# Optimization experiments

Hardware: AMD Instinct MI355X
Metric: run time of the kernel (lower is better)

## Reference

```python
import jax, jax.numpy as jnp
import numpy as np

STRIDES = [8, 16, 32, 64, 128]
HW = [(100, 128), (50, 64), (25, 32), (13, 16), (7, 8)]
SCORE_THR = 0.05
IOU_THR = 0.6
MAX_DET = 1000
MAX_OUT = 100  # fixed pad size in _post_process


def _coords(h, w, stride):
    # FCOS coords_fmap2orig: center of each cell in original image coords
    sx = jnp.arange(w, dtype=jnp.float32) * stride + stride // 2
    sy = jnp.arange(h, dtype=jnp.float32) * stride + stride // 2
    yy, xx = jnp.meshgrid(sy, sx, indexing='ij')
    return jnp.stack([xx.reshape(-1), yy.reshape(-1)], axis=-1)  # [h*w, 2]


def _reshape_cat(feats):
    # list of [B,C,h,w] -> [B, sum(h*w), C]
    outs = [f.transpose(0, 2, 3, 1).reshape(f.shape[0], -1, f.shape[1]) for f in feats]
    return jnp.concatenate(outs, axis=1)


def _nms_single(scores, classes, boxes):
    # scores [N] (sorted desc), classes [N] int, boxes [N,4]; greedy DIoU-NMS
    N = scores.shape[0]
    valid = scores >= SCORE_THR
    # batched_nms: offset boxes by class so cross-class boxes never overlap
    max_coord = jnp.max(jnp.where(valid[:, None], boxes, -jnp.inf))
    offs = classes.astype(boxes.dtype) * (max_coord + 1.0)
    b = boxes + offs[:, None]
    x1, y1, x2, y2 = b[:, 0], b[:, 1], b[:, 2], b[:, 3]
    areas = (x2 - x1 + 1.0) * (y2 - y1 + 1.0)
    cx, cy = (x1 + x2) * 0.5, (y1 + y2) * 0.5
    xmin = jnp.maximum(x1[:, None], x1[None, :]); ymin = jnp.maximum(y1[:, None], y1[None, :])
    xmax = jnp.minimum(x2[:, None], x2[None, :]); ymax = jnp.minimum(y2[:, None], y2[None, :])
    inter = jnp.clip(xmax - xmin, 0) * jnp.clip(ymax - ymin, 0)
    iou = inter / (areas[:, None] + areas[None, :] - inter)
    inter_diag = (cx[:, None] - cx[None, :]) ** 2 + (cy[:, None] - cy[None, :]) ** 2
    oxmin = jnp.minimum(x1[:, None], x1[None, :]); oymin = jnp.minimum(y1[:, None], y1[None, :])
    oxmax = jnp.maximum(x2[:, None], x2[None, :]); oymax = jnp.maximum(y2[:, None], y2[None, :])
    outer_diag = (oxmax - oxmin) ** 2 + (oymax - oymin) ** 2
    diou = iou - inter_diag / jnp.maximum(outer_diag, 1e-12)
    idxs = jnp.arange(N)

    def body(i, keep):
        sup = keep[i] & (idxs > i) & (diou[i] > IOU_THR)
        return keep & (~sup)

    keep = jax.lax.fori_loop(0, N, body, valid)
    # kept boxes in descending-score order, padded with -2 to MAX_OUT
    rank = jnp.cumsum(keep) - 1
    pos = jnp.where(keep, jnp.minimum(rank, MAX_OUT), MAX_OUT)  # slot MAX_OUT is dumped
    out_s = jnp.full((MAX_OUT + 1,), -2.0, scores.dtype).at[pos].set(jnp.where(keep, scores, -2.0))[:MAX_OUT]
    out_c = jnp.full((MAX_OUT + 1,), -2, classes.dtype).at[pos].set(jnp.where(keep, classes, -2))[:MAX_OUT]
    out_b = jnp.full((MAX_OUT + 1, 4), -2.0, boxes.dtype).at[pos].set(jnp.where(keep[:, None], boxes, -2.0))[:MAX_OUT]
    return out_s, out_c, out_b


def _forward(cls_feats, reg_feats):
    cls_logits = _reshape_cat(cls_feats)          # [B, L, C]
    reg_preds = _reshape_cat(reg_feats)           # [B, L, 4]
    coords = jnp.concatenate([_coords(h, w, s) for (h, w), s in zip(HW, STRIDES)], axis=0)
    cls_preds = jax.nn.sigmoid(cls_logits)
    cls_scores = jnp.max(cls_preds, axis=-1)      # [B, L]
    cls_classes = jnp.argmax(cls_preds, axis=-1) + 1
    x1y1 = coords[None] - reg_preds[..., :2]
    x2y2 = coords[None] + reg_preds[..., 2:]
    boxes = jnp.concatenate([x1y1, x2y2], axis=-1)  # [B, L, 4]
    max_num = min(MAX_DET, cls_scores.shape[-1])
    topv, topi = jax.lax.top_k(cls_scores, max_num)  # sorted descending
    top_c = jnp.take_along_axis(cls_classes, topi, axis=1)
    top_b = jnp.take_along_axis(boxes, topi[..., None], axis=1)
    return jax.vmap(_nms_single)(topv, top_c, top_b)


def setup_inputs() -> dict:
    key = jax.random.key(0)
    ks = jax.random.split(key, 16)
    inp = {}
    C = 80
    for i, (h, w) in enumerate(HW):
        inp[f'cls{i}'] = jax.random.normal(ks[i], (16, C, h, w), dtype=jnp.float32)
        # ltrb offsets scaled so boxes are realistically sized and overlap
        inp[f'reg{i}'] = jax.random.uniform(ks[5 + i], (16, 4, h, w), dtype=jnp.float32) * 64.0
    inp['boxes_anchor'] = jax.random.normal(ks[10], (16, 100, 4), dtype=jnp.float32)
    inp['labels_anchor'] = jax.random.randint(ks[11], (16, 100), 0, 80)
    inp['score_anchor'] = jax.random.uniform(ks[12], (16, 100), dtype=jnp.float32)
    return inp


def reference(cls0, cls1, cls2, cls3, cls4, reg0, reg1, reg2, reg3, reg4,
              boxes_anchor, labels_anchor, score_anchor):
    # nms_anchor (boxes_anchor, labels_anchor, score_anchor) is consumed but
    # does not affect the output in the original forward.
    scores, classes, boxes = _forward([cls0, cls1, cls2, cls3, cls4],
                                      [reg0, reg1, reg2, reg3, reg4])
    return scores, classes, boxes
```

## Files before the change

kernel.cpp:

```cpp
#include <hip/hip_runtime.h>
#include <math.h>

typedef unsigned int u32;
typedef unsigned long long u64;

#define BB 16
#define NANCH 17064
#define NGRP 4266
#define NTOP 1000
#define NWORD 16
#define NOUT 100
#define NBIN 8192
#define NSPLIT 17

__device__ __forceinline__ u32 fmap(float v) {
    u32 u = __float_as_uint(v);
    return (u & 0x80000000u) ? ~u : (u | 0x80000000u);
}
__device__ __forceinline__ float funmap(u32 u) {
    u32 b = (u & 0x80000000u) ? (u & 0x7FFFFFFFu) : ~u;
    return __uint_as_float(b);
}

__global__ void __launch_bounds__(256) k_anchor(
        const float* __restrict__ c0, const float* __restrict__ c1,
        const float* __restrict__ c2, const float* __restrict__ c3,
        const float* __restrict__ c4,
        const float* __restrict__ r0, const float* __restrict__ r1,
        const float* __restrict__ r2, const float* __restrict__ r3,
        const float* __restrict__ r4,
        u32* __restrict__ akey, int* __restrict__ aclass,
        float* __restrict__ abox) {
    int tid = threadIdx.x;
    int b = blockIdx.y;
    int gt = blockIdx.x * 256 + tid;
    if (gt >= 4 * NGRP) return;
    int p = gt >> 2, cs = gt & 3;
    int a = p * 4;

    const float *cp, *rp;
    int loc, wl, h, stride, half;
    if (a < 12800)      { loc = a;         wl = 7; h = 100; stride = 8;   half = 4;  cp = c0; rp = r0; }
    else if (a < 16000) { loc = a - 12800; wl = 6; h = 50;  stride = 16;  half = 8;  cp = c1; rp = r1; }
    else if (a < 16800) { loc = a - 16000; wl = 5; h = 25;  stride = 32;  half = 16; cp = c2; rp = r2; }
    else if (a < 17008) { loc = a - 16800; wl = 4; h = 13;  stride = 64;  half = 32; cp = c3; rp = r3; }
    else                { loc = a - 17008; wl = 3; h = 7;   stride = 128; half = 64; cp = c4; rp = r4; }
    int y = loc >> wl, x = loc & ((1 << wl) - 1);
    int hw = h << wl, hwq = hw >> 2;

    const float4* cb4 = (const float4*)(cp + (size_t)b * 80 * hw +
                                        (size_t)cs * 20 * hw + loc);
    int cbase = cs * 20;
    float4 v = cb4[0];
    float m0 = v.x, m1 = v.y, m2 = v.z, m3 = v.w;
    int a0 = cbase, a1 = cbase, a2 = cbase, a3 = cbase;
#pragma unroll
    for (int c = 1; c < 20; ++c) {
        float4 u = cb4[(size_t)c * hwq];
        int cc = cbase + c;
        if (u.x > m0) { m0 = u.x; a0 = cc; }
        if (u.y > m1) { m1 = u.y; a1 = cc; }
        if (u.z > m2) { m2 = u.z; a2 = cc; }
        if (u.w > m3) { m3 = u.w; a3 = cc; }
    }
    {
        bool low = (cs & 1) == 0;
        float pm; int pa; bool tk;
        pm = __shfl_xor(m0, 1); pa = __shfl_xor(a0, 1);
        tk = low ? (m0 >= pm) : (m0 > pm); m0 = tk ? m0 : pm; a0 = tk ? a0 : pa;
        pm = __shfl_xor(m1, 1); pa = __shfl_xor(a1, 1);
        tk = low ? (m1 >= pm) : (m1 > pm); m1 = tk ? m1 : pm; a1 = tk ? a1 : pa;
        pm = __shfl_xor(m2, 1); pa = __shfl_xor(a2, 1);
        tk = low ? (m2 >= pm) : (m2 > pm); m2 = tk ? m2 : pm; a2 = tk ? a2 : pa;
        pm = __shfl_xor(m3, 1); pa = __shfl_xor(a3, 1);
        tk = low ? (m3 >= pm) : (m3 > pm); m3 = tk ? m3 : pm; a3 = tk ? a3 : pa;
    }
    {
        bool low = (cs & 2) == 0;
        float pm; int pa; bool tk;
        pm = __shfl_xor(m0, 2); pa = __shfl_xor(a0, 2);
        tk = low ? (m0 >= pm) : (m0 > pm); m0 = tk ? m0 : pm; a0 = tk ? a0 : pa;
        pm = __shfl_xor(m1, 2); pa = __shfl_xor(a1, 2);
        tk = low ? (m1 >= pm) : (m1 > pm); m1 = tk ? m1 : pm; a1 = tk ? a1 : pa;
        pm = __shfl_xor(m2, 2); pa = __shfl_xor(a2, 2);
        tk = low ? (m2 >= pm) : (m2 > pm); m2 = tk ? m2 : pm; a2 = tk ? a2 : pa;
        pm = __shfl_xor(m3, 2); pa = __shfl_xor(a3, 2);
        tk = low ? (m3 >= pm) : (m3 > pm); m3 = tk ? m3 : pm; a3 = tk ? a3 : pa;
    }
    if (cs == 0) {
        const float4* rb4 = (const float4*)(rp + (size_t)b * 4 * hw + loc);
        float4 gl = rb4[0], gt_ = rb4[hwq], gr = rb4[2 * hwq], gb = rb4[3 * hwq];

        int idx = b * NANCH + a;
        *(uint4*)(akey + idx) = make_uint4(fmap(m0), fmap(m1), fmap(m2), fmap(m3));
        *(int4*)(aclass + idx) = make_int4(a0 + 1, a1 + 1, a2 + 1, a3 + 1);
        float cy = (float)(y * stride + half);
        float cx0 = (float)(x * stride + half);
        float gls[4] = {gl.x, gl.y, gl.z, gl.w};
        float gts[4] = {gt_.x, gt_.y, gt_.z, gt_.w};
        float grs[4] = {gr.x, gr.y, gr.z, gr.w};
        float gbs[4] = {gb.x, gb.y, gb.z, gb.w};
#pragma unroll
        for (int k = 0; k < 4; ++k) {
            float cx = cx0 + (float)(k * stride);
            *(float4*)(abox + (size_t)(idx + k) * 4) =
                make_float4(cx - gls[k], cy - gts[k], cx + grs[k], cy + gbs[k]);
        }
    }
}

__global__ void __launch_bounds__(256) k_hist(const u32* __restrict__ akey,
                                              u32* __restrict__ ghist) {
    __shared__ u32 lh[NBIN];
    int b = blockIdx.y, s = blockIdx.x, t = threadIdx.x;
    for (int i = t; i < NBIN; i += 256) lh[i] = 0;
    __syncthreads();
    int base = s * 1024;
    int n = min(1024, NANCH - base);
    if (4 * t < n) {
        uint4 k4 = *(const uint4*)(akey + (size_t)b * NANCH + base + 4 * t);
        atomicAdd(&lh[k4.x >> 19], 1u);
        atomicAdd(&lh[k4.y >> 19], 1u);
        atomicAdd(&lh[k4.z >> 19], 1u);
        atomicAdd(&lh[k4.w >> 19], 1u);
    }
    __syncthreads();
    u32* gh = ghist + b * NBIN;
    for (int i = t; i < NBIN; i += 256) {
        u32 c = lh[i];
        if (c) atomicAdd(&gh[i], c);
    }
}

__global__ void __launch_bounds__(256) k_compact(const u32* __restrict__ akey,
                                                 const u32* __restrict__ ghist,
                                                 u32* __restrict__ ccnt,
                                                 u64* __restrict__ cand) {
    __shared__ u32 hist[NBIN];
    __shared__ u32 seg[256];
    __shared__ u32 Ts, lcnt, baseoff;
    int b = blockIdx.y, s = blockIdx.x, t = threadIdx.x;
    const u32* gh = ghist + b * NBIN;
    for (int i = t; i < NBIN; i += 256) hist[i] = gh[i];
    if (t == 0) lcnt = 0;
    __syncthreads();
    u32 sg = 0;
#pragma unroll
    for (int j = 0; j < 32; ++j) sg += hist[t * 32 + ((j + t) & 31)];
    seg[t] = sg;
    __syncthreads();
    if (t == 0) {
        u32 acc = 0;
        int Tv = 0;
        for (int g = 255; g >= 0; --g) {
            if (acc + seg[g] >= NTOP) {
                for (int bin = g * 32 + 31; bin >= g * 32; --bin) {
                    acc += hist[bin];
                    if (acc >= NTOP) { Tv = bin; break; }
                }
                break;
            }
            acc += seg[g];
        }
        Ts = (u32)Tv;
    }
    __syncthreads();
    u32 T = Ts;

    int base = s * 1024;
    int n = min(1024, NANCH - base);
    u32 kk[4]; u32 pos[4]; bool m[4] = {false, false, false, false};
    if (4 * t < n) {
        uint4 k4 = *(const uint4*)(akey + (size_t)b * NANCH + base + 4 * t);
        kk[0] = k4.x; kk[1] = k4.y; kk[2] = k4.z; kk[3] = k4.w;
#pragma unroll
        for (int i = 0; i < 4; ++i) {
            m[i] = (kk[i] >> 19) >= T;
            if (m[i]) pos[i] = atomicAdd(&lcnt, 1u);
        }
    }
    __syncthreads();
    if (t == 0) baseoff = atomicAdd(&ccnt[b], lcnt);
    __syncthreads();
    u32 bo = baseoff;
    u64* cb = cand + (size_t)b * NANCH;
#pragma unroll
    for (int i = 0; i < 4; ++i) {
        if (m[i])
            cb[bo + pos[i]] =
                ((u64)kk[i] << 32) | (u64)(0xFFFFFFFFu - (u32)(base + 4 * t + i));
    }
}

__global__ void __launch_bounds__(256) k_rank(
        const u64* __restrict__ cand, const u32* __restrict__ ccnt,
        const int* __restrict__ aclass, const float* __restrict__ abox,
        float* __restrict__ tscore, int* __restrict__ tclass,
        float* __restrict__ tbox, u32* __restrict__ maxcU) {
    __shared__ u64 tile[2048];
    int b = blockIdx.y, tid = threadIdx.x;
    int C = (int)ccnt[b];
    const u64* ck = cand + (size_t)b * NANCH;
    for (int base = blockIdx.x * 256; base < C; base += gridDim.x * 256) {
        int i = base + tid;
        bool have = i < C;
        u64 my = have ? ck[i] : 0ull;
        int rank = 0;
        for (int t0 = 0; t0 < C; t0 += 2048) {
            int nt = min(2048, C - t0);
            __syncthreads();
            for (int j = tid; j < nt; j += 256) tile[j] = ck[t0 + j];
            __syncthreads();
            int r0 = 0, r1 = 0, r2 = 0, r3 = 0, r4 = 0, r5 = 0, r6 = 0, r7 = 0;
            int j = 0;
            for (; j + 8 <= nt; j += 8) {
                u64 v0 = tile[j + 0], v1 = tile[j + 1];
                u64 v2 = tile[j + 2], v3 = tile[j + 3];
                u64 v4 = tile[j + 4], v5 = tile[j + 5];
                u64 v6 = tile[j + 6], v7 = tile[j + 7];
                r0 += v0 > my; r1 += v1 > my; r2 += v2 > my; r3 += v3 > my;
                r4 += v4 > my; r5 += v5 > my; r6 += v6 > my; r7 += v7 > my;
            }
            for (; j < nt; ++j) r0 += tile[j] > my;
            rank += ((r0 + r1) + (r2 + r3)) + ((r4 + r5) + (r6 + r7));
        }
        u32 mymax = 0;
        if (have && rank < NTOP) {
            u32 a = 0xFFFFFFFFu - (u32)(my & 0xFFFFFFFFull);
            int src = b * NANCH + (int)a;
            int dst = b * NTOP + rank;
            float logit = funmap((u32)(my >> 32));
            float sc = 1.0f / (1.0f + expf(-logit));
            float b0 = abox[src * 4 + 0], b1 = abox[src * 4 + 1];
            float b2 = abox[src * 4 + 2], b3 = abox[src * 4 + 3];
            tscore[dst] = sc;
            tclass[dst] = aclass[src];
            tbox[dst * 4 + 0] = b0;
            tbox[dst * 4 + 1] = b1;
            tbox[dst * 4 + 2] = b2;
            tbox[dst * 4 + 3] = b3;
            if (sc >= 0.05f)
                mymax = fmap(fmaxf(fmaxf(b0, b1), fmaxf(b2, b3)));
        }
        for (int off = 32; off > 0; off >>= 1) {
            u32 o = (u32)__shfl_down((int)mymax, off);
            mymax = mymax > o ? mymax : o;
        }
        if ((tid & 63) == 0) atomicMax(&maxcU[b], mymax);
    }
}

__global__ void k_sup(const float* __restrict__ tbox, const int* __restrict__ tclass,
                      const u32* __restrict__ maxcU, u64* __restrict__ sup) {
    int u = blockIdx.x, b = blockIdx.y;
    int ti = 0, rem = u;
    while (rem >= NWORD - ti) { rem -= NWORD - ti; ++ti; }
    int tj = ti + rem;
    int t = threadIdx.x;
    __shared__ double jx1[64], jy1[64], jx2[64], jy2[64], jcx[64], jcy[64], jar[64];
    double mc1 = (double)funmap(maxcU[b]) + 1.0;
    int j = tj * 64 + t;
    if (j < NTOP) {
        const float* bx = tbox + (size_t)(b * NTOP + j) * 4;
        double o = (double)tclass[b * NTOP + j] * mc1;
        double x1 = (double)bx[0] + o, y1 = (double)bx[1] + o;
        double x2 = (double)bx[2] + o, y2 = (double)bx[3] + o;
        jx1[t] = x1; jy1[t] = y1; jx2[t] = x2; jy2[t] = y2;
        jcx[t] = (x1 + x2) * 0.5; jcy[t] = (y1 + y2) * 0.5;
        jar[t] = (x2 - x1 + 1.0) * (y2 - y1 + 1.0);
    }
    __syncthreads();
    int i = ti * 64 + t;
    if (i >= NTOP) return;
    const float* bx = tbox + (size_t)(b * NTOP + i) * 4;
    double o = (double)tclass[b * NTOP + i] * mc1;
    double ix1 = (double)bx[0] + o, iy1 = (double)bx[1] + o;
    double ix2 = (double)bx[2] + o, iy2 = (double)bx[3] + o;
    double icx = (ix1 + ix2) * 0.5, icy = (iy1 + iy2) * 0.5;
    double iar = (ix2 - ix1 + 1.0) * (iy2 - iy1 + 1.0);
    u64 bits = 0;
    int jbase = tj * 64;
    for (int jj = 0; jj < 64; ++jj) {
        int jg = jbase + jj;
        if (jg >= NTOP) break;
        if (jg <= i) continue;
        double xm = fmax(ix1, jx1[jj]), ym = fmax(iy1, jy1[jj]);
        double xM = fmin(ix2, jx2[jj]), yM = fmin(iy2, jy2[jj]);
        double inter = fmax(xM - xm, 0.0) * fmax(yM - ym, 0.0);
        double iou = inter / (iar + jar[jj] - inter);
        double dx = icx - jcx[jj], dy = icy - jcy[jj];
        double idg = dx * dx + dy * dy;
        double ox = fmax(ix2, jx2[jj]) - fmin(ix1, jx1[jj]);
        double oy = fmax(iy2, jy2[jj]) - fmin(iy1, jy1[jj]);
        double odg = ox * ox + oy * oy;
        double diou = iou - idg / fmax(odg, 1e-12);
        if (diou > 0.6) bits |= (1ull << jj);
    }
    sup[(size_t)(b * NTOP + i) * NWORD + tj] = bits;
}

__global__ void __launch_bounds__(64) k_scan(
        const u64* __restrict__ sup, const float* __restrict__ tscore,
        const int* __restrict__ tclass, const float* __restrict__ tbox,
        float* __restrict__ out) {
    int b = blockIdx.x, lane = threadIdx.x;
    __shared__ u64 lds[64 * 17];
    __shared__ int kept_lds[NOUT];
    const u64* supb = sup + (size_t)b * NTOP * NWORD;
    u64 remw = 0;
    int kept = 0;
    for (int t = 0; t < NWORD; ++t) {
        int r0 = t * 64;
#pragma unroll
        for (int q = 0; q < 16; ++q) {
            int e = q * 64 + lane;
            int rr = r0 + (e >> 4), w = e & 15;
            u64 v = (rr < NTOP) ? supb[(size_t)rr * 16 + w] : 0ull;
            lds[(e >> 4) * 17 + w] = v;
        }
        __syncthreads();
        int r = r0 + lane;
        float s = (r < NTOP) ? tscore[b * NTOP + r] : -1.0f;
        u64 vmask = __ballot(s >= 0.05f);
        u64 M = lds[lane * 17 + t];
        u64 rem_t = __shfl(remw, t);
        u64 cand = vmask & ~rem_t;
        u64 keepmask = 0;
        while (cand) {
            int k = __ffsll(cand) - 1;
            keepmask |= 1ull << k;
            if (lane == 0) kept_lds[kept] = r0 + k;
            ++kept;
            if (kept >= NOUT) break;
            u64 Mk = __shfl(M, k);
            cand &= ~(Mk | (1ull << k));
        }
        if (lane < NWORD) {
            u64 km = keepmask;
            while (km) {
                int k = __ffsll(km) - 1;
                km &= km - 1;
                remw |= lds[k * 17 + lane];
            }
        }
        __syncthreads();
        if (kept >= NOUT) break;
    }
    float* os = out + b * NOUT;
    float* oc = out + BB * NOUT + b * NOUT;
    float* ob = out + 2 * BB * NOUT + (size_t)b * NOUT * 4;
    for (int i = lane; i < NOUT; i += 64) { os[i] = -2.0f; oc[i] = -2.0f; }
    for (int i = lane; i < NOUT * 4; i += 64) ob[i] = -2.0f;
    __syncthreads();
    int ncopy = kept < NOUT ? kept : NOUT;
    for (int r = lane; r < ncopy; r += 64) {
        int i = kept_lds[r];
        os[r] = tscore[b * NTOP + i];
        oc[r] = (float)tclass[b * NTOP + i];
        ob[r * 4 + 0] = tbox[(size_t)(b * NTOP + i) * 4 + 0];
        ob[r * 4 + 1] = tbox[(size_t)(b * NTOP + i) * 4 + 1];
        ob[r * 4 + 2] = tbox[(size_t)(b * NTOP + i) * 4 + 2];
        ob[r * 4 + 3] = tbox[(size_t)(b * NTOP + i) * 4 + 3];
    }
}

extern "C" void kernel_launch(void* const* d_in, const int* in_sizes, int n_in,
                              void* d_out, int out_size, void* d_ws, size_t ws_size,
                              hipStream_t stream) {
    (void)in_sizes; (void)n_in; (void)out_size; (void)ws_size;
    const float* cls[5];
    const float* reg[5];
    for (int i = 0; i < 5; ++i) {
        cls[i] = (const float*)d_in[2 * i];
        reg[i] = (const float*)d_in[2 * i + 1];
    }
    float* out = (float*)d_out;

    char* ws = (char*)d_ws;
    u32* ghist = (u32*)ws;           ws += (size_t)BB * NBIN * sizeof(u32);
    u32* ccnt = (u32*)ws;            ws += 64;
    u32* maxcU = (u32*)ws;           ws += 64;
    size_t zbytes = (size_t)BB * NBIN * sizeof(u32) + 128;
    u64* cand = (u64*)ws;            ws += (size_t)BB * NANCH * sizeof(u64);
    u64* sup = (u64*)ws;             ws += (size_t)BB * NTOP * NWORD * sizeof(u64);
    u32* akey = (u32*)ws;            ws += (size_t)BB * NANCH * sizeof(u32);
    int* aclass = (int*)ws;          ws += (size_t)BB * NANCH * sizeof(int);
    float* abox = (float*)ws;        ws += (size_t)BB * NANCH * 4 * sizeof(float);
    float* tscore = (float*)ws;      ws += (size_t)BB * NTOP * sizeof(float);
    int* tclass = (int*)ws;          ws += (size_t)BB * NTOP * sizeof(int);
    float* tbox = (float*)ws;        ws += (size_t)BB * NTOP * 4 * sizeof(float);

    hipMemsetAsync(ghist, 0, zbytes, stream);

    k_anchor<<<dim3((4 * NGRP + 255) / 256, BB), 256, 0, stream>>>(
        cls[0], cls[1], cls[2], cls[3], cls[4],
        reg[0], reg[1], reg[2], reg[3], reg[4],
        akey, aclass, abox);
    k_hist<<<dim3(NSPLIT, BB), 256, 0, stream>>>(akey, ghist);
    k_compact<<<dim3(NSPLIT, BB), 256, 0, stream>>>(akey, ghist, ccnt, cand);
    k_rank<<<dim3(8, BB), 256, 0, stream>>>(cand, ccnt, aclass, abox,
                                            tscore, tclass, tbox, maxcU);
    k_sup<<<dim3(136, BB), 64, 0, stream>>>(tbox, tclass, maxcU, sup);
    k_scan<<<BB, 64, 0, stream>>>(sup, tscore, tclass, tbox, out);
}
```

Measured before the change: 235.3 us.

## Defer class argmax and box decode to top-K anchors; add two-level radix select

The anchor kernel now computes only the max logit per anchor. The argmax class and the box decode are recomputed in k_rank, and only for the top-1000 survivors, by re-reading the inputs. A new refinement pass builds a second-level histogram on the threshold bin so compaction keeps close to exactly 1000 candidates instead of a whole coarse bin. This removes the per-anchor class and box writes and shrinks the candidates the O(n^2) rank has to process. The cost is an extra kernel launch and scattered input reads for the survivors, and the equality-based argmax must match the reference's tie-breaking.

```diff
diff --git a/kernel.cpp b/kernel.cpp
--- a/kernel.cpp
+++ b/kernel.cpp
@@ -22,15 +22,27 @@
     return __uint_as_float(b);
 }
 
+__device__ __forceinline__ void decode_level(
+        int a, const float* c0, const float* c1, const float* c2,
+        const float* c3, const float* c4,
+        const float* r0, const float* r1, const float* r2,
+        const float* r3, const float* r4,
+        const float*& cp, const float*& rp,
+        int& loc, int& wl, int& hw, int& stride, int& half) {
+    int h;
+    if (a < 12800)      { loc = a;         wl = 7; h = 100; stride = 8;   half = 4;  cp = c0; rp = r0; }
+    else if (a < 16000) { loc = a - 12800; wl = 6; h = 50;  stride = 16;  half = 8;  cp = c1; rp = r1; }
+    else if (a < 16800) { loc = a - 16000; wl = 5; h = 25;  stride = 32;  half = 16; cp = c2; rp = r2; }
+    else if (a < 17008) { loc = a - 16800; wl = 4; h = 13;  stride = 64;  half = 32; cp = c3; rp = r3; }
+    else                { loc = a - 17008; wl = 3; h = 7;   stride = 128; half = 64; cp = c4; rp = r4; }
+    hw = h << wl;
+}
+
 __global__ void __launch_bounds__(256) k_anchor(
         const float* __restrict__ c0, const float* __restrict__ c1,
         const float* __restrict__ c2, const float* __restrict__ c3,
         const float* __restrict__ c4,
-        const float* __restrict__ r0, const float* __restrict__ r1,
-        const float* __restrict__ r2, const float* __restrict__ r3,
-        const float* __restrict__ r4,
-        u32* __restrict__ akey, int* __restrict__ aclass,
-        float* __restrict__ abox) {
+        u32* __restrict__ akey) {
     int tid = threadIdx.x;
     int b = blockIdx.y;
     int gt = blockIdx.x * 256 + tid;
@@ -38,74 +50,35 @@
     int p = gt >> 2, cs = gt & 3;
     int a = p * 4;
 
-    const float *cp, *rp;
-    int loc, wl, h, stride, half;
-    if (a < 12800)      { loc = a;         wl = 7; h = 100; stride = 8;   half = 4;  cp = c0; rp = r0; }
-    else if (a < 16000) { loc = a - 12800; wl = 6; h = 50;  stride = 16;  half = 8;  cp = c1; rp = r1; }
-    else if (a < 16800) { loc = a - 16000; wl = 5; h = 25;  stride = 32;  half = 16; cp = c2; rp = r2; }
-    else if (a < 17008) { loc = a - 16800; wl = 4; h = 13;  stride = 64;  half = 32; cp = c3; rp = r3; }
-    else                { loc = a - 17008; wl = 3; h = 7;   stride = 128; half = 64; cp = c4; rp = r4; }
-    int y = loc >> wl, x = loc & ((1 << wl) - 1);
-    int hw = h << wl, hwq = hw >> 2;
+    const float* cp;
+    int loc, wl, h, hw;
+    if (a < 12800)      { loc = a;         wl = 7; h = 100; cp = c0; }
+    else if (a < 16000) { loc = a - 12800; wl = 6; h = 50;  cp = c1; }
+    else if (a < 16800) { loc = a - 16000; wl = 5; h = 25;  cp = c2; }
+    else if (a < 17008) { loc = a - 16800; wl = 4; h = 13;  cp = c3; }
+    else                { loc = a - 17008; wl = 3; h = 7;   cp = c4; }
+    hw = h << wl;
+    int hwq = hw >> 2;
 
     const float4* cb4 = (const float4*)(cp + (size_t)b * 80 * hw +
                                         (size_t)cs * 20 * hw + loc);
-    int cbase = cs * 20;
     float4 v = cb4[0];
     float m0 = v.x, m1 = v.y, m2 = v.z, m3 = v.w;
-    int a0 = cbase, a1 = cbase, a2 = cbase, a3 = cbase;
 #pragma unroll
     for (int c = 1; c < 20; ++c) {
         float4 u = cb4[(size_t)c * hwq];
-        int cc = cbase + c;
-        if (u.x > m0) { m0 = u.x; a0 = cc; }
-        if (u.y > m1) { m1 = u.y; a1 = cc; }
-        if (u.z > m2) { m2 = u.z; a2 = cc; }
-        if (u.w > m3) { m3 = u.w; a3 = cc; }
-    }
-    {
-        bool low = (cs & 1) == 0;
-        float pm; int pa; bool tk;
-        pm = __shfl_xor(m0, 1); pa = __shfl_xor(a0, 1);
-        tk = low ? (m0 >= pm) : (m0 > pm); m0 = tk ? m0 : pm; a0 = tk ? a0 : pa;
-        pm = __shfl_xor(m1, 1); pa = __shfl_xor(a1, 1);
-        tk = low ? (m1 >= pm) : (m1 > pm); m1 = tk ? m1 : pm; a1 = tk ? a1 : pa;
-        pm = __shfl_xor(m2, 1); pa = __shfl_xor(a2, 1);
-        tk = low ? (m2 >= pm) : (m2 > pm); m2 = tk ? m2 : pm; a2 = tk ? a2 : pa;
-        pm = __shfl_xor(m3, 1); pa = __shfl_xor(a3, 1);
-        tk = low ? (m3 >= pm) : (m3 > pm); m3 = tk ? m3 : pm; a3 = tk ? a3 : pa;
-    }
-    {
-        bool low = (cs & 2) == 0;
-        float pm; int pa; bool tk;
-        pm = __shfl_xor(m0, 2); pa = __shfl_xor(a0, 2);
-        tk = low ? (m0 >= pm) : (m0 > pm); m0 = tk ? m0 : pm; a0 = tk ? a0 : pa;
-        pm = __shfl_xor(m1, 2); pa = __shfl_xor(a1, 2);
-        tk = low ? (m1 >= pm) : (m1 > pm); m1 = tk ? m1 : pm; a1 = tk ? a1 : pa;
-        pm = __shfl_xor(m2, 2); pa = __shfl_xor(a2, 2);
-        tk = low ? (m2 >= pm) : (m2 > pm); m2 = tk ? m2 : pm; a2 = tk ? a2 : pa;
-        pm = __shfl_xor(m3, 2); pa = __shfl_xor(a3, 2);
-        tk = low ? (m3 >= pm) : (m3 > pm); m3 = tk ? m3 : pm; a3 = tk ? a3 : pa;
-    }
+        m0 = fmaxf(m0, u.x);
+        m1 = fmaxf(m1, u.y);
+        m2 = fmaxf(m2, u.z);
+        m3 = fmaxf(m3, u.w);
+    }
+    m0 = fmaxf(m0, __shfl_xor(m0, 1)); m1 = fmaxf(m1, __shfl_xor(m1, 1));
+    m2 = fmaxf(m2, __shfl_xor(m2, 1)); m3 = fmaxf(m3, __shfl_xor(m3, 1));
+    m0 = fmaxf(m0, __shfl_xor(m0, 2)); m1 = fmaxf(m1, __shfl_xor(m1, 2));
+    m2 = fmaxf(m2, __shfl_xor(m2, 2)); m3 = fmaxf(m3, __shfl_xor(m3, 2));
     if (cs == 0) {
-        const float4* rb4 = (const float4*)(rp + (size_t)b * 4 * hw + loc);
-        float4 gl = rb4[0], gt_ = rb4[hwq], gr = rb4[2 * hwq], gb = rb4[3 * hwq];
-
         int idx = b * NANCH + a;
         *(uint4*)(akey + idx) = make_uint4(fmap(m0), fmap(m1), fmap(m2), fmap(m3));
-        *(int4*)(aclass + idx) = make_int4(a0 + 1, a1 + 1, a2 + 1, a3 + 1);
-        float cy = (float)(y * stride + half);
-        float cx0 = (float)(x * stride + half);
-        float gls[4] = {gl.x, gl.y, gl.z, gl.w};
-        float gts[4] = {gt_.x, gt_.y, gt_.z, gt_.w};
-        float grs[4] = {gr.x, gr.y, gr.z, gr.w};
-        float gbs[4] = {gb.x, gb.y, gb.z, gb.w};
-#pragma unroll
-        for (int k = 0; k < 4; ++k) {
-            float cx = cx0 + (float)(k * stride);
-            *(float4*)(abox + (size_t)(idx + k) * 4) =
-                make_float4(cx - gls[k], cy - gts[k], cx + grs[k], cy + gbs[k]);
-        }
     }
 }
 
@@ -132,18 +105,77 @@
     }
 }
 
+__global__ void __launch_bounds__(256) k_refine(const u32* __restrict__ akey,
+                                                const u32* __restrict__ ghist,
+                                                u32* __restrict__ ghist2,
+                                                u32* __restrict__ Tn) {
+    __shared__ u32 hist[NBIN];
+    __shared__ u32 seg[256];
+    __shared__ u32 Ts;
+    int b = blockIdx.y, s = blockIdx.x, t = threadIdx.x;
+    const u32* gh = ghist + b * NBIN;
+    for (int i = t; i < NBIN; i += 256) hist[i] = gh[i];
+    __syncthreads();
+    u32 sg = 0;
+#pragma unroll
+    for (int j = 0; j < 32; ++j) sg += hist[t * 32 + ((j + t) & 31)];
+    seg[t] = sg;
+    __syncthreads();
+    if (t == 0) {
+        u32 acc = 0;
+        int Tv = 0;
+        u32 nAbove = 0;
+        for (int g = 255; g >= 0; --g) {
+            if (acc + seg[g] >= NTOP) {
+                for (int bin = g * 32 + 31; bin >= g * 32; --bin) {
+                    u32 h = hist[bin];
+                    if (acc + h >= NTOP) { Tv = bin; nAbove = acc; break; }
+                    acc += h;
+                }
+                break;
+            }
+            acc += seg[g];
+        }
+        Ts = (u32)Tv;
+        Tn[b * 2 + 0] = (u32)Tv;
+        Tn[b * 2 + 1] = NTOP - nAbove;
+    }
+    __syncthreads();
+    u32 T = Ts;
+    for (int i = t; i < NBIN; i += 256) hist[i] = 0;
+    __syncthreads();
+    int base = s * 1024;
+    int n = min(1024, NANCH - base);
+    if (4 * t < n) {
+        uint4 k4 = *(const uint4*)(akey + (size_t)b * NANCH + base + 4 * t);
+        u32 kk[4] = {k4.x, k4.y, k4.z, k4.w};
+#pragma unroll
+        for (int i = 0; i < 4; ++i)
+            if ((kk[i] >> 19) == T) atomicAdd(&hist[(kk[i] >> 6) & 8191u], 1u);
+    }
+    __syncthreads();
+    u32* gh2 = ghist2 + b * NBIN;
+    for (int i = t; i < NBIN; i += 256) {
+        u32 c = hist[i];
+        if (c) atomicAdd(&gh2[i], c);
+    }
+}
+
 __global__ void __launch_bounds__(256) k_compact(const u32* __restrict__ akey,
-                                                 const u32* __restrict__ ghist,
+                                                 const u32* __restrict__ ghist2,
+                                                 const u32* __restrict__ Tn,
                                                  u32* __restrict__ ccnt,
                                                  u64* __restrict__ cand) {
     __shared__ u32 hist[NBIN];
     __shared__ u32 seg[256];
-    __shared__ u32 Ts, lcnt, baseoff;
+    __shared__ u32 T2s, lcnt, baseoff;
     int b = blockIdx.y, s = blockIdx.x, t = threadIdx.x;
-    const u32* gh = ghist + b * NBIN;
-    for (int i = t; i < NBIN; i += 256) hist[i] = gh[i];
+    const u32* gh2 = ghist2 + b * NBIN;
+    for (int i = t; i < NBIN; i += 256) hist[i] = gh2[i];
     if (t == 0) lcnt = 0;
     __syncthreads();
+    u32 T = Tn[b * 2 + 0];
+    u32 need = Tn[b * 2 + 1];
     u32 sg = 0;
 #pragma unroll
     for (int j = 0; j < 32; ++j) sg += hist[t * 32 + ((j + t) & 31)];
@@ -153,19 +185,19 @@
         u32 acc = 0;
         int Tv = 0;
         for (int g = 255; g >= 0; --g) {
-            if (acc + seg[g] >= NTOP) {
+            if (acc + seg[g] >= need) {
                 for (int bin = g * 32 + 31; bin >= g * 32; --bin) {
                     acc += hist[bin];
-                    if (acc >= NTOP) { Tv = bin; break; }
+                    if (acc >= need) { Tv = bin; break; }
                 }
                 break;
             }
             acc += seg[g];
         }
-        Ts = (u32)Tv;
-    }
-    __syncthreads();
-    u32 T = Ts;
+        T2s = (u32)Tv;
+    }
+    __syncthreads();
+    u32 T2 = T2s;
 
     int base = s * 1024;
     int n = min(1024, NANCH - base);
@@ -175,7 +207,8 @@
         kk[0] = k4.x; kk[1] = k4.y; kk[2] = k4.z; kk[3] = k4.w;
 #pragma unroll
         for (int i = 0; i < 4; ++i) {
-            m[i] = (kk[i] >> 19) >= T;
+            u32 hi = kk[i] >> 19;
+            m[i] = (hi > T) || (hi == T && ((kk[i] >> 6) & 8191u) >= T2);
             if (m[i]) pos[i] = atomicAdd(&lcnt, 1u);
         }
     }
@@ -194,7 +227,12 @@
 
 __global__ void __launch_bounds__(256) k_rank(
         const u64* __restrict__ cand, const u32* __restrict__ ccnt,
-        const int* __restrict__ aclass, const float* __restrict__ abox,
+        const float* __restrict__ c0, const float* __restrict__ c1,
+        const float* __restrict__ c2, const float* __restrict__ c3,
+        const float* __restrict__ c4,
+        const float* __restrict__ r0, const float* __restrict__ r1,
+        const float* __restrict__ r2, const float* __restrict__ r3,
+        const float* __restrict__ r4,
         float* __restrict__ tscore, int* __restrict__ tclass,
         float* __restrict__ tbox, u32* __restrict__ maxcU) {
     __shared__ u64 tile[2048];
@@ -211,30 +249,46 @@
             __syncthreads();
             for (int j = tid; j < nt; j += 256) tile[j] = ck[t0 + j];
             __syncthreads();
-            int r0 = 0, r1 = 0, r2 = 0, r3 = 0, r4 = 0, r5 = 0, r6 = 0, r7 = 0;
+            int q0 = 0, q1 = 0, q2 = 0, q3 = 0, q4 = 0, q5 = 0, q6 = 0, q7 = 0;
             int j = 0;
             for (; j + 8 <= nt; j += 8) {
                 u64 v0 = tile[j + 0], v1 = tile[j + 1];
                 u64 v2 = tile[j + 2], v3 = tile[j + 3];
                 u64 v4 = tile[j + 4], v5 = tile[j + 5];
                 u64 v6 = tile[j + 6], v7 = tile[j + 7];
-                r0 += v0 > my; r1 += v1 > my; r2 += v2 > my; r3 += v3 > my;
-                r4 += v4 > my; r5 += v5 > my; r6 += v6 > my; r7 += v7 > my;
+                q0 += v0 > my; q1 += v1 > my; q2 += v2 > my; q3 += v3 > my;
+                q4 += v4 > my; q5 += v5 > my; q6 += v6 > my; q7 += v7 > my;
             }
-            for (; j < nt; ++j) r0 += tile[j] > my;
-            rank += ((r0 + r1) + (r2 + r3)) + ((r4 + r5) + (r6 + r7));
+            for (; j < nt; ++j) q0 += tile[j] > my;
+            rank += ((q0 + q1) + (q2 + q3)) + ((q4 + q5) + (q6 + q7));
         }
         u32 mymax = 0;
         if (have && rank < NTOP) {
-            u32 a = 0xFFFFFFFFu - (u32)(my & 0xFFFFFFFFull);
-            int src = b * NANCH + (int)a;
+            int a = (int)(0xFFFFFFFFu - (u32)(my & 0xFFFFFFFFull));
+            const float* cp; const float* rp;
+            int loc, wl, hw, stride, half;
+            decode_level(a, c0, c1, c2, c3, c4, r0, r1, r2, r3, r4,
+                         cp, rp, loc, wl, hw, stride, half);
+            int y = loc >> wl, x = loc & ((1 << wl) - 1);
+            float mlogit = funmap((u32)(my >> 32));
+            const float* cb = cp + (size_t)b * 80 * hw + loc;
+            int arg = 100;
+            for (int cc0 = 0; cc0 < 80 && arg == 100; cc0 += 16) {
+                float v[16];
+#pragma unroll
+                for (int j = 0; j < 16; ++j) v[j] = cb[(size_t)(cc0 + j) * hw];
+#pragma unroll
+                for (int j = 0; j < 16; ++j)
+                    if (v[j] == mlogit && arg == 100) arg = cc0 + j;
+            }
+            const float* rb = rp + (size_t)b * 4 * hw + loc;
+            float g0 = rb[0], g1 = rb[hw], g2 = rb[2 * hw], g3 = rb[3 * hw];
+            float cx = (float)(x * stride + half), cy = (float)(y * stride + half);
+            float b0 = cx - g0, b1 = cy - g1, b2 = cx + g2, b3 = cy + g3;
+            float sc = 1.0f / (1.0f + expf(-mlogit));
             int dst = b * NTOP + rank;
-            float logit = funmap((u32)(my >> 32));
-            float sc = 1.0f / (1.0f + expf(-logit));
-            float b0 = abox[src * 4 + 0], b1 = abox[src * 4 + 1];
-            float b2 = abox[src * 4 + 2], b3 = abox[src * 4 + 3];
             tscore[dst] = sc;
-            tclass[dst] = aclass[src];
+            tclass[dst] = arg + 1;
             tbox[dst * 4 + 0] = b0;
             tbox[dst * 4 + 1] = b1;
             tbox[dst * 4 + 2] = b2;
@@ -324,16 +378,16 @@
         u64 vmask = __ballot(s >= 0.05f);
         u64 M = lds[lane * 17 + t];
         u64 rem_t = __shfl(remw, t);
-        u64 cand = vmask & ~rem_t;
+        u64 cnd = vmask & ~rem_t;
         u64 keepmask = 0;
-        while (cand) {
-            int k = __ffsll(cand) - 1;
+        while (cnd) {
+            int k = __ffsll(cnd) - 1;
             keepmask |= 1ull << k;
             if (lane == 0) kept_lds[kept] = r0 + k;
             ++kept;
             if (kept >= NOUT) break;
             u64 Mk = __shfl(M, k);
-            cand &= ~(Mk | (1ull << k));
+            cnd &= ~(Mk | (1ull << k));
         }
         if (lane < NWORD) {
             u64 km = keepmask;
@@ -378,14 +432,14 @@
 
     char* ws = (char*)d_ws;
     u32* ghist = (u32*)ws;           ws += (size_t)BB * NBIN * sizeof(u32);
+    u32* ghist2 = (u32*)ws;          ws += (size_t)BB * NBIN * sizeof(u32);
     u32* ccnt = (u32*)ws;            ws += 64;
     u32* maxcU = (u32*)ws;           ws += 64;
-    size_t zbytes = (size_t)BB * NBIN * sizeof(u32) + 128;
+    size_t zbytes = (size_t)2 * BB * NBIN * sizeof(u32) + 128;
+    u32* Tn = (u32*)ws;              ws += 128;
     u64* cand = (u64*)ws;            ws += (size_t)BB * NANCH * sizeof(u64);
     u64* sup = (u64*)ws;             ws += (size_t)BB * NTOP * NWORD * sizeof(u64);
     u32* akey = (u32*)ws;            ws += (size_t)BB * NANCH * sizeof(u32);
-    int* aclass = (int*)ws;          ws += (size_t)BB * NANCH * sizeof(int);
-    float* abox = (float*)ws;        ws += (size_t)BB * NANCH * 4 * sizeof(float);
     float* tscore = (float*)ws;      ws += (size_t)BB * NTOP * sizeof(float);
     int* tclass = (int*)ws;          ws += (size_t)BB * NTOP * sizeof(int);
     float* tbox = (float*)ws;        ws += (size_t)BB * NTOP * 4 * sizeof(float);
@@ -393,13 +447,15 @@
     hipMemsetAsync(ghist, 0, zbytes, stream);
 
     k_anchor<<<dim3((4 * NGRP + 255) / 256, BB), 256, 0, stream>>>(
+        cls[0], cls[1], cls[2], cls[3], cls[4], akey);
+    k_hist<<<dim3(NSPLIT, BB), 256, 0, stream>>>(akey, ghist);
+    k_refine<<<dim3(NSPLIT, BB), 256, 0, stream>>>(akey, ghist, ghist2, Tn);
+    k_compact<<<dim3(NSPLIT, BB), 256, 0, stream>>>(akey, ghist2, Tn, ccnt, cand);
+    k_rank<<<dim3(8, BB), 256, 0, stream>>>(
+        cand, ccnt,
         cls[0], cls[1], cls[2], cls[3], cls[4],
         reg[0], reg[1], reg[2], reg[3], reg[4],
-        akey, aclass, abox);
-    k_hist<<<dim3(NSPLIT, BB), 256, 0, stream>>>(akey, ghist);
-    k_compact<<<dim3(NSPLIT, BB), 256, 0, stream>>>(akey, ghist, ccnt, cand);
-    k_rank<<<dim3(8, BB), 256, 0, stream>>>(cand, ccnt, aclass, abox,
-                                            tscore, tclass, tbox, maxcU);
+        tscore, tclass, tbox, maxcU);
     k_sup<<<dim3(136, BB), 64, 0, stream>>>(tbox, tclass, maxcU, sup);
     k_scan<<<BB, 64, 0, stream>>>(sup, tscore, tclass, tbox, out);
 }
```

Result: slower. 259.8 us (+10.4%).
